# Performance work log

Hardware: AMD Instinct MI355X
Metric: run time of the kernel (lower is better)

Reference implementation:

```python
import jax, jax.numpy as jnp
import numpy as np

N_NODES = 100000
N_EDGES = 3200000
D_FEAT = 128
N_CLASSES = 8


def setup_inputs() -> dict:
    key = jax.random.key(0)
    ks = jax.random.split(key, 8)
    x = jax.random.normal(ks[0], (N_NODES, D_FEAT), dtype=jnp.float32)
    edge_index = jax.random.randint(ks[1], (2, N_EDGES), 0, N_NODES, dtype=jnp.int64)
    W1 = jax.random.normal(ks[2], (D_FEAT, 32), dtype=jnp.float32) / np.sqrt(D_FEAT)
    b1 = jnp.zeros((32,), dtype=jnp.float32)
    W2 = jax.random.normal(ks[3], (32, 16), dtype=jnp.float32) / np.sqrt(32)
    b2 = jnp.zeros((16,), dtype=jnp.float32)
    Wc = jax.random.normal(ks[4], (16, N_CLASSES), dtype=jnp.float32) / np.sqrt(16)
    bc = jnp.zeros((N_CLASSES,), dtype=jnp.float32)
    return {"x": x, "edge_index": edge_index, "W1": W1, "b1": b1,
            "W2": W2, "b2": b2, "Wc": Wc, "bc": bc}


def _gcn_conv(h, src, dst, norm, W, b, num_nodes):
    # PyG GCNConv: linear transform, then sym-normalized scatter-add, then bias
    h = h @ W                                   # [N, out]
    msg = h[src] * norm[:, None]                # [E+N, out] gather + scale
    out = jax.ops.segment_sum(msg, dst, num_segments=num_nodes)
    return out + b


def reference(x, edge_index, W1, b1, W2, b2, Wc, bc):
    num_nodes = x.shape[0]
    loop = jnp.arange(num_nodes, dtype=edge_index.dtype)
    src = jnp.concatenate([edge_index[0], loop])  # add self-loops (PyG default)
    dst = jnp.concatenate([edge_index[1], loop])
    deg = jax.ops.segment_sum(jnp.ones_like(dst, dtype=x.dtype), dst,
                              num_segments=num_nodes)
    dinv = jnp.where(deg > 0, jax.lax.rsqrt(deg), 0.0)
    norm = dinv[src] * dinv[dst]                # symmetric normalization per edge

    h = _gcn_conv(x, src, dst, norm, W1, b1, num_nodes)
    h = jax.nn.relu(h)
    # dropout p=0.5 is identity in eval mode (training=False)
    h = _gcn_conv(h, src, dst, norm, W2, b2, num_nodes)
    h = jax.nn.relu(h)
    logits = h @ Wc + bc
    return jax.nn.log_softmax(logits, axis=1)
```

## Files before the change

kernel.cpp:

```cpp
#include <hip/hip_runtime.h>
#include <math.h>

#define N_NODES 100000
#define N_EDGES 3200000
#define D_FEAT 128
#define H1 32
#define H2 16
#define NC 8

#define NBUCK 391
#define BCAP 12288
#define HCAP 6144
#define EPB 4096
#define EPT 8
#define NSB ((N_EDGES + EPB - 1) / EPB)

#define P_NODES 32
#define P_CAP 3072

typedef short s16x8 __attribute__((ext_vector_type(8)));
typedef float f32x4 __attribute__((ext_vector_type(4)));

__device__ inline unsigned short f2bf(float f) {
    unsigned int u = __float_as_uint(f);
    u += 0x7FFF + ((u >> 16) & 1);
    return (unsigned short)(u >> 16);
}
__device__ inline float bf2f(unsigned short h) {
    return __uint_as_float((unsigned int)h << 16);
}

__device__ inline int wave_scan_incl(int v, int lane) {
#pragma unroll
    for (int off = 1; off < 64; off <<= 1) {
        const int t = __shfl_up(v, off, 64);
        if (lane >= off) v += t;
    }
    return v;
}


__global__ __launch_bounds__(512) void k_pre(const int* __restrict__ ei,
                                             const float* __restrict__ x,
                                             const float* __restrict__ W1,
                                             int* __restrict__ bucket_cursor,
                                             int* __restrict__ ebuf,
                                             unsigned short* __restrict__ y16) {
    __shared__ union {
        struct {
            int hist[NBUCK], lofs[NBUCK], rank[NBUCK], gb[NBUCK], wsum[8], is64;
            int pay[EPB];
            unsigned short pbk[EPB];
        } sc;
        struct {
            unsigned short wf[2 * 4 * 64 * 8];
            float os[8][16][33];
        } gm;
    } u;
    const int tid = threadIdx.x;
    const int lane = tid & 63;
    const int wid = tid >> 6;

    if (blockIdx.x >= NSB) {
        const int gb_ = blockIdx.x - NSB;
        for (int idx = tid; idx < 2 * 4 * 64 * 8; idx += 512) {
            const int j  = idx & 7;
            const int ln = (idx >> 3) & 63;
            const int kk = (idx >> 9) & 3;
            const int nt = idx >> 11;
            const int k = kk * 32 + ((ln >> 4) << 3) + j;
            const int n = nt * 16 + (ln & 15);
            u.gm.wf[idx] = f2bf(W1[k * H1 + n]);
        }
        __syncthreads();
        const int w = tid >> 6;
        const int m = lane & 15;
        const int quad = lane >> 4;
        const int rl = lane >> 2;
        const int seg = lane & 3;
        const s16x8* bf = (const s16x8*)u.gm.wf;
#pragma unroll
        for (int t = 0; t < 2; ++t) {
            const int row0 = (gb_ << 8) + (w * 2 + t) * 16;
            const bool act = (row0 < N_NODES);
            if (act) {
                f32x4 acc0 = {0.f, 0.f, 0.f, 0.f};
                f32x4 acc1 = {0.f, 0.f, 0.f, 0.f};
#pragma unroll
                for (int kk = 0; kk < 4; ++kk) {
                    const float* xp = x + (size_t)(row0 + m) * D_FEAT + kk * 32 + quad * 8;
                    const float4 p0 = ((const float4*)xp)[0];
                    const float4 p1 = ((const float4*)xp)[1];
                    s16x8 a;
                    a[0] = (short)f2bf(p0.x); a[1] = (short)f2bf(p0.y);
                    a[2] = (short)f2bf(p0.z); a[3] = (short)f2bf(p0.w);
                    a[4] = (short)f2bf(p1.x); a[5] = (short)f2bf(p1.y);
                    a[6] = (short)f2bf(p1.z); a[7] = (short)f2bf(p1.w);
                    acc0 = __builtin_amdgcn_mfma_f32_16x16x32_bf16(a, bf[kk * 64 + lane], acc0, 0, 0, 0);
                    acc1 = __builtin_amdgcn_mfma_f32_16x16x32_bf16(a, bf[(4 + kk) * 64 + lane], acc1, 0, 0, 0);
                }
#pragma unroll
                for (int r = 0; r < 4; ++r) {
                    u.gm.os[w][quad * 4 + r][m]      = acc0[r];
                    u.gm.os[w][quad * 4 + r][16 + m] = acc1[r];
                }
            }
            __syncthreads();
            if (act) {
                const int row = row0 + rl;
                const float* p = &u.gm.os[w][rl][seg * 8];
                uint4 o;
                o.x = (unsigned int)f2bf(p[0]) | ((unsigned int)f2bf(p[1]) << 16);
                o.y = (unsigned int)f2bf(p[2]) | ((unsigned int)f2bf(p[3]) << 16);
                o.z = (unsigned int)f2bf(p[4]) | ((unsigned int)f2bf(p[5]) << 16);
                o.w = (unsigned int)f2bf(p[6]) | ((unsigned int)f2bf(p[7]) << 16);
                *(uint4*)(y16 + (size_t)row * 32 + seg * 8) = o;
            }
            __syncthreads();
        }
        return;
    }

    for (int i = tid; i < NBUCK; i += 512) { u.sc.hist[i] = 0; u.sc.rank[i] = 0; }
    if (tid < 64) {
        int v = ei[2 * tid + 1];
#pragma unroll
        for (int off = 1; off < 64; off <<= 1) v |= __shfl_xor(v, off, 64);
        if (tid == 0) u.sc.is64 = (v == 0) ? 1 : 0;
    }
    __syncthreads();
    const int e0 = blockIdx.x * EPB;
    const int n = min(EPB, N_EDGES - e0);
    const bool is64 = (u.sc.is64 != 0);
    int rs[EPT], rd[EPT];
    if (is64) {
#pragma unroll
        for (int k = 0; k < EPT / 2; ++k) {
            const int i = 2 * (tid + k * 512);
            if (i < n) {
                const int e = e0 + i;
                const int4 s = *(const int4*)&ei[2 * e];
                const int4 d = *(const int4*)&ei[2 * N_EDGES + 2 * e];
                rs[2 * k] = s.x; rs[2 * k + 1] = s.z;
                rd[2 * k] = d.x; rd[2 * k + 1] = d.z;
                atomicAdd(&u.sc.hist[d.x >> 8], 1);
                atomicAdd(&u.sc.hist[d.z >> 8], 1);
            }
        }
    } else {
#pragma unroll
        for (int k = 0; k < EPT / 2; ++k) {
            const int i = 2 * (tid + k * 512);
            if (i < n) {
                const int e = e0 + i;
                const int2 s = *(const int2*)&ei[e];
                const int2 d = *(const int2*)&ei[N_EDGES + e];
                rs[2 * k] = s.x; rs[2 * k + 1] = s.y;
                rd[2 * k] = d.x; rd[2 * k + 1] = d.y;
                atomicAdd(&u.sc.hist[d.x >> 8], 1);
                atomicAdd(&u.sc.hist[d.y >> 8], 1);
            }
        }
    }
    __syncthreads();
    const int own = (tid < NBUCK) ? u.sc.hist[tid] : 0;
    int incl = wave_scan_incl(own, lane);
    if (lane == 63) u.sc.wsum[wid] = incl;
    __syncthreads();
    if (tid == 0) {
        int r = 0;
#pragma unroll
        for (int w = 0; w < 8; ++w) { const int t = u.sc.wsum[w]; u.sc.wsum[w] = r; r += t; }
    }
    __syncthreads();
    incl += u.sc.wsum[wid];
    if (tid < NBUCK) {
        u.sc.lofs[tid] = incl - own;
        if (own > 0) u.sc.gb[tid] = tid * BCAP + atomicAdd(&bucket_cursor[tid], own);
    }
    __syncthreads();
#pragma unroll
    for (int k = 0; k < EPT / 2; ++k) {
        const int i = 2 * (tid + k * 512);
        if (i < n) {
#pragma unroll
            for (int j = 0; j < 2; ++j) {
                const int b = rd[2 * k + j] >> 8;
                const int p = u.sc.lofs[b] + atomicAdd(&u.sc.rank[b], 1);
                u.sc.pay[p] = (rs[2 * k + j] << 8) | (rd[2 * k + j] & 255);
                u.sc.pbk[p] = (unsigned short)b;
            }
        }
    }
    __syncthreads();
    for (int p = tid; p < n; p += 512) {
        const int b = u.sc.pbk[p];
        ebuf[u.sc.gb[b] + (p - u.sc.lofs[b])] = u.sc.pay[p];
    }
}


__global__ __launch_bounds__(512) void k_mid(const int* __restrict__ ebuf,
                                             const int* __restrict__ bucket_cursor,
                                             const unsigned short* __restrict__ y16,
                                             int* __restrict__ degc,
                                             float* __restrict__ dinv,
                                             unsigned int* __restrict__ u1q) {
    __shared__ int cnt[256];
    const int b = blockIdx.x;
    const int tid = threadIdx.x;
    if (tid < 256) cnt[tid] = 0;
    __syncthreads();
    const int nb = bucket_cursor[b];
    const int rb = b * BCAP;
    for (int i = tid; i < nb; i += 512)
        atomicAdd(&cnt[ebuf[rb + i] & 255], 1);
    __syncthreads();
    if (tid < 256) {
        const int v = (b << 8) + tid;
        const int cn = cnt[tid];
        degc[v] = cn;
        if (v < N_NODES) {
            const float dv = rsqrtf(1.0f + (float)cn);
            dinv[v] = dv;
            unsigned int r[16];
            const uint4* yp = (const uint4*)(y16 + (size_t)v * 32);
            *(uint4*)&r[0]  = yp[0];
            *(uint4*)&r[4]  = yp[1];
            *(uint4*)&r[8]  = yp[2];
            *(uint4*)&r[12] = yp[3];
            unsigned int wq[8];
#pragma unroll
            for (int j = 0; j < 8; ++j) {
                const float c0 = bf2f((unsigned short)r[2 * j]) * dv;
                const float c1 = bf2f((unsigned short)(r[2 * j] >> 16)) * dv;
                const float c2 = bf2f((unsigned short)r[2 * j + 1]) * dv;
                const float c3 = bf2f((unsigned short)(r[2 * j + 1] >> 16)) * dv;
                unsigned int pk = __builtin_amdgcn_cvt_pk_fp8_f32(c0, c1, 0u, false);
                wq[j] = __builtin_amdgcn_cvt_pk_fp8_f32(c2, c3, pk, true);
            }
            uint4 oa; oa.x = wq[0]; oa.y = wq[1]; oa.z = wq[2]; oa.w = wq[3];
            uint4 ob; ob.x = wq[4]; ob.y = wq[5]; ob.z = wq[6]; ob.w = wq[7];
            ((uint4*)u1q)[(size_t)v * 2]     = oa;
            ((uint4*)u1q)[(size_t)v * 2 + 1] = ob;
        }
    }
}


#define ACC8(Q) do { \
    a0 += __builtin_amdgcn_cvt_f32_fp8((Q).x, 0); \
    a1 += __builtin_amdgcn_cvt_f32_fp8((Q).x, 1); \
    a2 += __builtin_amdgcn_cvt_f32_fp8((Q).x, 2); \
    a3 += __builtin_amdgcn_cvt_f32_fp8((Q).x, 3); \
    a4 += __builtin_amdgcn_cvt_f32_fp8((Q).y, 0); \
    a5 += __builtin_amdgcn_cvt_f32_fp8((Q).y, 1); \
    a6 += __builtin_amdgcn_cvt_f32_fp8((Q).y, 2); \
    a7 += __builtin_amdgcn_cvt_f32_fp8((Q).y, 3); \
} while (0)

__global__ __launch_bounds__(512) void k_fuse1(const int* __restrict__ ebuf,
                                               const int* __restrict__ bucket_cursor,
                                               const int* __restrict__ degc,
                                               const unsigned int* __restrict__ u1q,
                                               const float* __restrict__ b1,
                                               const float* __restrict__ W2,
                                               int* __restrict__ row_ptr,
                                               int* __restrict__ col_idx,
                                               unsigned int* __restrict__ u2b) {
    __shared__ int srt[HCAP];
    __shared__ int cnt[256];
    __shared__ int cur[256];
    __shared__ int wsum[8];
    __shared__ int wsum2[4];
    __shared__ float Ws[H1 * H2];
    __shared__ float hs[128][33];
    __shared__ int s_wb, s_base, s_nh;
    const int b = blockIdx.x >> 1;
    const int h = blockIdx.x & 1;
    const int tid = threadIdx.x;
    const int lane = tid & 63;
    const int wid = tid >> 6;
    if (tid < 256) cnt[tid] = degc[(b << 8) + tid];
    for (int i = tid; i < H1 * H2; i += 512) Ws[i] = W2[i];
    const int own0 = (tid < NBUCK) ? bucket_cursor[tid] : 0;
    int incl0 = wave_scan_incl(own0, lane);
    if (lane == 63) wsum[wid] = incl0;
    __syncthreads();
    if (tid == 0) {
        int r = 0;
#pragma unroll
        for (int w = 0; w < 8; ++w) { const int t = wsum[w]; wsum[w] = r; r += t; }
    }
    __syncthreads();
    if (tid == b) s_wb = incl0 + wsum[wid] - own0;
    const int nb = bucket_cursor[b];
    const int rb = b * BCAP;
    int ownc = 0, inclc = 0;
    if (tid < 256) {
        ownc = cnt[tid];
        inclc = wave_scan_incl(ownc, lane);
        if (lane == 63) wsum2[wid] = inclc;
    }
    __syncthreads();
    if (tid == 0) {
        int r = 0;
#pragma unroll
        for (int w = 0; w < 4; ++w) { const int t = wsum2[w]; wsum2[w] = r; r += t; }
    }
    __syncthreads();
    const int wb = s_wb;
    if (tid < 256) {
        inclc += wsum2[wid];
        const int excl = inclc - ownc;
        cur[tid] = excl;
        const int v = (b << 8) + tid;
        if (v <= N_NODES) row_ptr[v] = wb + excl;
    }
    __syncthreads();
    if (tid == 0) {
        s_base = cur[h * 128];
        s_nh = (h ? nb : cur[128]) - cur[h * 128];
    }
    __syncthreads();
    const int base_h = s_base;
    const int nh = s_nh;
    for (int i = tid; i < nb; i += 512) {
        const int pk = ebuf[rb + i];
        const int dl = pk & 255;
        if ((dl >> 7) == h) {
            const int slot = atomicAdd(&cur[dl], 1);
            srt[slot - base_h] = pk >> 8;
        }
    }
    __syncthreads();
    for (int i = tid; i < nh; i += 512)
        col_idx[wb + base_h + i] = srt[i];
    const int nnl = tid >> 2;
    const int lq = tid & 3;
    const int nn = h * 128 + nnl;
    const int v = (b << 8) + nn;
    if (v < N_NODES) {
        const uint2* base = (const uint2*)u1q;
        const uint2 q = base[(size_t)v * 4 + lq];
        float a0 = __builtin_amdgcn_cvt_f32_fp8(q.x, 0);
        float a1 = __builtin_amdgcn_cvt_f32_fp8(q.x, 1);
        float a2 = __builtin_amdgcn_cvt_f32_fp8(q.x, 2);
        float a3 = __builtin_amdgcn_cvt_f32_fp8(q.x, 3);
        float a4 = __builtin_amdgcn_cvt_f32_fp8(q.y, 0);
        float a5 = __builtin_amdgcn_cvt_f32_fp8(q.y, 1);
        float a6 = __builtin_amdgcn_cvt_f32_fp8(q.y, 2);
        float a7 = __builtin_amdgcn_cvt_f32_fp8(q.y, 3);
        const int cn = cnt[nn];
        const int e = cur[nn] - base_h;
        int j = e - cn;
        for (; j + 7 < e; j += 8) {
            const int s0 = srt[j + 0];
            const int s1 = srt[j + 1];
            const int s2 = srt[j + 2];
            const int s3 = srt[j + 3];
            const int s4 = srt[j + 4];
            const int s5 = srt[j + 5];
            const int s6 = srt[j + 6];
            const int s7 = srt[j + 7];
            const uint2 q0 = base[(size_t)s0 * 4 + lq];
            const uint2 q1 = base[(size_t)s1 * 4 + lq];
            const uint2 q2 = base[(size_t)s2 * 4 + lq];
            const uint2 q3 = base[(size_t)s3 * 4 + lq];
            const uint2 q4 = base[(size_t)s4 * 4 + lq];
            const uint2 q5 = base[(size_t)s5 * 4 + lq];
            const uint2 q6 = base[(size_t)s6 * 4 + lq];
            const uint2 q7 = base[(size_t)s7 * 4 + lq];
            ACC8(q0); ACC8(q1); ACC8(q2); ACC8(q3);
            ACC8(q4); ACC8(q5); ACC8(q6); ACC8(q7);
        }
        for (; j + 3 < e; j += 4) {
            const int s0 = srt[j + 0];
            const int s1 = srt[j + 1];
            const int s2 = srt[j + 2];
            const int s3 = srt[j + 3];
            const uint2 q0 = base[(size_t)s0 * 4 + lq];
            const uint2 q1 = base[(size_t)s1 * 4 + lq];
            const uint2 q2 = base[(size_t)s2 * 4 + lq];
            const uint2 q3 = base[(size_t)s3 * 4 + lq];
            ACC8(q0); ACC8(q1); ACC8(q2); ACC8(q3);
        }
        for (; j < e; ++j) {
            const uint2 qq = base[(size_t)srt[j] * 4 + lq];
            ACC8(qq);
        }
        const float dv = rsqrtf(1.0f + (float)cn);
        const float4 bb0 = ((const float4*)b1)[lq * 2];
        const float4 bb1 = ((const float4*)b1)[lq * 2 + 1];
        float* hp = &hs[nnl][lq * 8];
        hp[0] = fmaxf(fmaf(a0, dv, bb0.x), 0.0f);
        hp[1] = fmaxf(fmaf(a1, dv, bb0.y), 0.0f);
        hp[2] = fmaxf(fmaf(a2, dv, bb0.z), 0.0f);
        hp[3] = fmaxf(fmaf(a3, dv, bb0.w), 0.0f);
        hp[4] = fmaxf(fmaf(a4, dv, bb1.x), 0.0f);
        hp[5] = fmaxf(fmaf(a5, dv, bb1.y), 0.0f);
        hp[6] = fmaxf(fmaf(a6, dv, bb1.z), 0.0f);
        hp[7] = fmaxf(fmaf(a7, dv, bb1.w), 0.0f);
        if (lq == 0) hs[nnl][32] = dv;
    }
    __syncthreads();
    {
        const int nn2 = tid >> 2;
        const int jq = tid & 3;
        const int v2 = (b << 8) + h * 128 + nn2;
        if (v2 < N_NODES) {
            const int j0 = jq * 4;
            const float dv = hs[nn2][32];
            float s0 = 0.f, s1 = 0.f, s2 = 0.f, s3 = 0.f;
#pragma unroll
            for (int k = 0; k < H1; ++k) {
                const float hk = hs[nn2][k];
                s0 = fmaf(hk, Ws[k * H2 + j0 + 0], s0);
                s1 = fmaf(hk, Ws[k * H2 + j0 + 1], s1);
                s2 = fmaf(hk, Ws[k * H2 + j0 + 2], s2);
                s3 = fmaf(hk, Ws[k * H2 + j0 + 3], s3);
            }
            uint2 o;
            o.x = (unsigned int)f2bf(s0 * dv) | ((unsigned int)f2bf(s1 * dv) << 16);
            o.y = (unsigned int)f2bf(s2 * dv) | ((unsigned int)f2bf(s3 * dv) << 16);
            ((uint2*)u2b)[(size_t)v2 * 4 + jq] = o;
        }
    }
}


#define ACC4(Q) do { \
    a0 += bf2f((unsigned short)(Q).x); \
    a1 += bf2f((unsigned short)((Q).x >> 16)); \
    a2 += bf2f((unsigned short)(Q).y); \
    a3 += bf2f((unsigned short)((Q).y >> 16)); \
} while (0)

__global__ __launch_bounds__(256) void k_pull2f(const int* __restrict__ row_ptr,
                                                const int* __restrict__ col_idx,
                                                const float* __restrict__ dinv,
                                                const unsigned int* __restrict__ u2b,
                                                const float* __restrict__ b2,
                                                const float* __restrict__ Wc,
                                                const float* __restrict__ bc,
                                                float* __restrict__ out) {
    __shared__ float hs[P_NODES][17];
    __shared__ float Wcs[H2 * NC];
    __shared__ float bcs[NC];
    __shared__ int lidx[P_CAP];
    const int tid = threadIdx.x;
    if (tid < H2 * NC) Wcs[tid] = Wc[tid];
    if (tid < NC) bcs[tid] = bc[tid];
    const int v0 = blockIdx.x * P_NODES;
    const int base_off = row_ptr[v0];
    const int range = row_ptr[v0 + P_NODES] - base_off;
    const bool ovf = (range > P_CAP);
    const int stg = ovf ? 0 : range;
    for (int j = tid; j < stg; j += 256) lidx[j] = col_idx[base_off + j];
    __syncthreads();
    const int n = tid >> 3;
    const int half = (tid >> 2) & 1;
    const int lq = tid & 3;
    const int v = v0 + n;
    const uint2* base = (const uint2*)u2b;
    float a0 = 0.f, a1 = 0.f, a2 = 0.f, a3 = 0.f;
    if (half == 0) {
        const uint2 q = base[(size_t)v * 4 + lq];
        a0 = bf2f((unsigned short)q.x); a1 = bf2f((unsigned short)(q.x >> 16));
        a2 = bf2f((unsigned short)q.y); a3 = bf2f((unsigned short)(q.y >> 16));
    }
    const int beg = row_ptr[v] - base_off;
    const int end = row_ptr[v + 1] - base_off;
    int i = beg + half;
    if (!ovf) {
        for (; i + 14 < end; i += 16) {
            const int s0 = lidx[i];
            const int s1 = lidx[i + 2];
            const int s2 = lidx[i + 4];
            const int s3 = lidx[i + 6];
            const int s4 = lidx[i + 8];
            const int s5 = lidx[i + 10];
            const int s6 = lidx[i + 12];
            const int s7 = lidx[i + 14];
            const uint2 q0 = base[(size_t)s0 * 4 + lq];
            const uint2 q1 = base[(size_t)s1 * 4 + lq];
            const uint2 q2 = base[(size_t)s2 * 4 + lq];
            const uint2 q3 = base[(size_t)s3 * 4 + lq];
            const uint2 q4 = base[(size_t)s4 * 4 + lq];
            const uint2 q5 = base[(size_t)s5 * 4 + lq];
            const uint2 q6 = base[(size_t)s6 * 4 + lq];
            const uint2 q7 = base[(size_t)s7 * 4 + lq];
            ACC4(q0); ACC4(q1); ACC4(q2); ACC4(q3);
            ACC4(q4); ACC4(q5); ACC4(q6); ACC4(q7);
        }
        for (; i + 6 < end; i += 8) {
            const int s0 = lidx[i];
            const int s1 = lidx[i + 2];
            const int s2 = lidx[i + 4];
            const int s3 = lidx[i + 6];
            const uint2 q0 = base[(size_t)s0 * 4 + lq];
            const uint2 q1 = base[(size_t)s1 * 4 + lq];
            const uint2 q2 = base[(size_t)s2 * 4 + lq];
            const uint2 q3 = base[(size_t)s3 * 4 + lq];
            ACC4(q0); ACC4(q1); ACC4(q2); ACC4(q3);
        }
        for (; i < end; i += 2) {
            const uint2 qq = base[(size_t)lidx[i] * 4 + lq];
            ACC4(qq);
        }
    } else {
        const int* gp = col_idx + base_off;
        for (; i + 14 < end; i += 16) {
            const int s0 = gp[i];
            const int s1 = gp[i + 2];
            const int s2 = gp[i + 4];
            const int s3 = gp[i + 6];
            const int s4 = gp[i + 8];
            const int s5 = gp[i + 10];
            const int s6 = gp[i + 12];
            const int s7 = gp[i + 14];
            const uint2 q0 = base[(size_t)s0 * 4 + lq];
            const uint2 q1 = base[(size_t)s1 * 4 + lq];
            const uint2 q2 = base[(size_t)s2 * 4 + lq];
            const uint2 q3 = base[(size_t)s3 * 4 + lq];
            const uint2 q4 = base[(size_t)s4 * 4 + lq];
            const uint2 q5 = base[(size_t)s5 * 4 + lq];
            const uint2 q6 = base[(size_t)s6 * 4 + lq];
            const uint2 q7 = base[(size_t)s7 * 4 + lq];
            ACC4(q0); ACC4(q1); ACC4(q2); ACC4(q3);
            ACC4(q4); ACC4(q5); ACC4(q6); ACC4(q7);
        }
        for (; i < end; i += 2) {
            const uint2 qq = base[(size_t)gp[i] * 4 + lq];
            ACC4(qq);
        }
    }
    a0 += __shfl_xor(a0, 4, 64); a1 += __shfl_xor(a1, 4, 64);
    a2 += __shfl_xor(a2, 4, 64); a3 += __shfl_xor(a3, 4, 64);
    if (half == 0) {
        const float dv = dinv[v];
        const float4 bb = ((const float4*)b2)[lq];
        float* hp = &hs[n][lq * 4];
        hp[0] = fmaxf(fmaf(a0, dv, bb.x), 0.0f);
        hp[1] = fmaxf(fmaf(a1, dv, bb.y), 0.0f);
        hp[2] = fmaxf(fmaf(a2, dv, bb.z), 0.0f);
        hp[3] = fmaxf(fmaf(a3, dv, bb.w), 0.0f);
    }
    __syncthreads();
    if (tid < P_NODES) {
        const int vv = v0 + tid;
        float lg[NC];
#pragma unroll
        for (int j = 0; j < NC; ++j) lg[j] = bcs[j];
#pragma unroll
        for (int k = 0; k < H2; ++k) {
            const float hk = hs[tid][k];
#pragma unroll
            for (int j = 0; j < NC; ++j)
                lg[j] = fmaf(hk, Wcs[k * NC + j], lg[j]);
        }
        float m = lg[0];
#pragma unroll
        for (int j = 1; j < NC; ++j) m = fmaxf(m, lg[j]);
        float s = 0.0f;
#pragma unroll
        for (int j = 0; j < NC; ++j) s += expf(lg[j] - m);
        const float lse = logf(s) + m;
        float4 o0, o1;
        o0.x = lg[0] - lse; o0.y = lg[1] - lse;
        o0.z = lg[2] - lse; o0.w = lg[3] - lse;
        o1.x = lg[4] - lse; o1.y = lg[5] - lse;
        o1.z = lg[6] - lse; o1.w = lg[7] - lse;
        float4* op = (float4*)(out + (size_t)vv * NC);
        op[0] = o0; op[1] = o1;
    }
}


extern "C" void kernel_launch(void* const* d_in, const int* in_sizes, int n_in,
                              void* d_out, int out_size, void* d_ws, size_t ws_size,
                              hipStream_t stream) {
    const float* x   = (const float*)d_in[0];
    const int*   ei  = (const int*)d_in[1];
    const float* W1  = (const float*)d_in[2];
    const float* b1  = (const float*)d_in[3];
    const float* W2  = (const float*)d_in[4];
    const float* b2  = (const float*)d_in[5];
    const float* Wc  = (const float*)d_in[6];
    const float* bc  = (const float*)d_in[7];
    float* out = (float*)d_out;

    int*   bucket_cursor = (int*)d_ws;
    float* dinv          = (float*)(bucket_cursor + 512);
    int*   degc          = (int*)dinv + 100000;
    int*   row_ptr       = degc + 100096;
    int*   col_idx       = row_ptr + 100016;
    unsigned int* u1q    = (unsigned int*)(col_idx + 3200000);
    unsigned int* u2b    = u1q + 800000;
    int*   ebuf          = (int*)(u2b + 800000);
    unsigned short* y16  = (unsigned short*)col_idx;

    hipMemsetAsync(bucket_cursor, 0, 512 * sizeof(int), stream);
    k_pre <<<NSB + NBUCK, 512, 0, stream>>>(ei, x, W1, bucket_cursor, ebuf, y16);
    k_mid <<<NBUCK, 512, 0, stream>>>(ebuf, bucket_cursor, y16, degc, dinv, u1q);
    k_fuse1<<<NBUCK * 2, 512, 0, stream>>>(ebuf, bucket_cursor, degc, u1q, b1, W2, row_ptr, col_idx, u2b);
    k_pull2f<<<N_NODES / P_NODES, 256, 0, stream>>>(row_ptr, col_idx, dinv, u2b, b2, Wc, bc, out);
}
```

Measured before the change: 201.9 us.

## Split destination buckets to 128 nodes and precompute bucket base offsets once

Edges are now binned into 782 buckets of 128 destination nodes instead of 391 buckets of 256. Each k_fuse1 block then reads only its own bucket, where before two half-blocks each scanned the full 256-node bucket and filtered. The global exclusive scan of bucket sizes moves into a single block of k_mid, replacing the redundant per-block scan in k_fuse1. The cost is a larger shared histogram and two-pass scan in k_pre, plus more scattered atomic bucket appends to global memory.

```diff
diff --git a/kernel.cpp b/kernel.cpp
--- a/kernel.cpp
+++ b/kernel.cpp
@@ -8,8 +8,8 @@
 #define H2 16
 #define NC 8
 
-#define NBUCK 391
-#define BCAP 12288
+#define NB2 782
+#define BCAP2 6144
 #define HCAP 6144
 #define EPB 4096
 #define EPT 8
@@ -48,7 +48,8 @@
                                              unsigned short* __restrict__ y16) {
     __shared__ union {
         struct {
-            int hist[NBUCK], lofs[NBUCK], rank[NBUCK], gb[NBUCK], wsum[8], is64;
+            int hist[NB2], lofs[NB2], rank[NB2], gb[NB2];
+            int wsumA[8], wsumB[8], tot, is64;
             int pay[EPB];
             unsigned short pbk[EPB];
         } sc;
@@ -121,7 +122,7 @@
         return;
     }
 
-    for (int i = tid; i < NBUCK; i += 512) { u.sc.hist[i] = 0; u.sc.rank[i] = 0; }
+    for (int i = tid; i < NB2; i += 512) { u.sc.hist[i] = 0; u.sc.rank[i] = 0; }
     if (tid < 64) {
         int v = ei[2 * tid + 1];
 #pragma unroll
@@ -143,8 +144,8 @@
                 const int4 d = *(const int4*)&ei[2 * N_EDGES + 2 * e];
                 rs[2 * k] = s.x; rs[2 * k + 1] = s.z;
                 rd[2 * k] = d.x; rd[2 * k + 1] = d.z;
-                atomicAdd(&u.sc.hist[d.x >> 8], 1);
-                atomicAdd(&u.sc.hist[d.z >> 8], 1);
+                atomicAdd(&u.sc.hist[d.x >> 7], 1);
+                atomicAdd(&u.sc.hist[d.z >> 7], 1);
             }
         }
     } else {
@@ -157,26 +158,40 @@
                 const int2 d = *(const int2*)&ei[N_EDGES + e];
                 rs[2 * k] = s.x; rs[2 * k + 1] = s.y;
                 rd[2 * k] = d.x; rd[2 * k + 1] = d.y;
-                atomicAdd(&u.sc.hist[d.x >> 8], 1);
-                atomicAdd(&u.sc.hist[d.y >> 8], 1);
+                atomicAdd(&u.sc.hist[d.x >> 7], 1);
+                atomicAdd(&u.sc.hist[d.y >> 7], 1);
             }
         }
     }
     __syncthreads();
-    const int own = (tid < NBUCK) ? u.sc.hist[tid] : 0;
-    int incl = wave_scan_incl(own, lane);
-    if (lane == 63) u.sc.wsum[wid] = incl;
+    const int own0 = u.sc.hist[tid];
+    int incl0 = wave_scan_incl(own0, lane);
+    if (lane == 63) u.sc.wsumA[wid] = incl0;
     __syncthreads();
     if (tid == 0) {
         int r = 0;
 #pragma unroll
-        for (int w = 0; w < 8; ++w) { const int t = u.sc.wsum[w]; u.sc.wsum[w] = r; r += t; }
-    }
-    __syncthreads();
-    incl += u.sc.wsum[wid];
-    if (tid < NBUCK) {
-        u.sc.lofs[tid] = incl - own;
-        if (own > 0) u.sc.gb[tid] = tid * BCAP + atomicAdd(&bucket_cursor[tid], own);
+        for (int w = 0; w < 8; ++w) { const int t = u.sc.wsumA[w]; u.sc.wsumA[w] = r; r += t; }
+        u.sc.tot = r;
+    }
+    __syncthreads();
+    incl0 += u.sc.wsumA[wid];
+    u.sc.lofs[tid] = incl0 - own0;
+    const int own1 = (tid < NB2 - 512) ? u.sc.hist[512 + tid] : 0;
+    int incl1 = wave_scan_incl(own1, lane);
+    if (lane == 63) u.sc.wsumB[wid] = incl1;
+    __syncthreads();
+    if (tid == 0) {
+        int r = 0;
+#pragma unroll
+        for (int w = 0; w < 8; ++w) { const int t = u.sc.wsumB[w]; u.sc.wsumB[w] = r; r += t; }
+    }
+    __syncthreads();
+    incl1 += u.sc.wsumB[wid] + u.sc.tot;
+    if (tid < NB2 - 512) u.sc.lofs[512 + tid] = incl1 - own1;
+    for (int i = tid; i < NB2; i += 512) {
+        const int ownI = u.sc.hist[i];
+        if (ownI > 0) u.sc.gb[i] = i * BCAP2 + atomicAdd(&bucket_cursor[i], ownI);
     }
     __syncthreads();
 #pragma unroll
@@ -185,7 +200,7 @@
         if (i < n) {
 #pragma unroll
             for (int j = 0; j < 2; ++j) {
-                const int b = rd[2 * k + j] >> 8;
+                const int b = rd[2 * k + j] >> 7;
                 const int p = u.sc.lofs[b] + atomicAdd(&u.sc.rank[b], 1);
                 u.sc.pay[p] = (rs[2 * k + j] << 8) | (rd[2 * k + j] & 255);
                 u.sc.pbk[p] = (unsigned short)b;
@@ -205,16 +220,23 @@
                                              const unsigned short* __restrict__ y16,
                                              int* __restrict__ degc,
                                              float* __restrict__ dinv,
+                                             int* __restrict__ bbase,
                                              unsigned int* __restrict__ u1q) {
     __shared__ int cnt[256];
+    __shared__ int wsA[8], wsB[8];
+    __shared__ int tt;
     const int b = blockIdx.x;
     const int tid = threadIdx.x;
     if (tid < 256) cnt[tid] = 0;
     __syncthreads();
-    const int nb = bucket_cursor[b];
-    const int rb = b * BCAP;
-    for (int i = tid; i < nb; i += 512)
-        atomicAdd(&cnt[ebuf[rb + i] & 255], 1);
+#pragma unroll
+    for (int j = 0; j < 2; ++j) {
+        const int b2 = 2 * b + j;
+        const int nbj = bucket_cursor[b2];
+        const int rbj = b2 * BCAP2;
+        for (int i = tid; i < nbj; i += 512)
+            atomicAdd(&cnt[ebuf[rbj + i] & 255], 1);
+    }
     __syncthreads();
     if (tid < 256) {
         const int v = (b << 8) + tid;
@@ -245,6 +267,34 @@
             ((uint4*)u1q)[(size_t)v * 2 + 1] = ob;
         }
     }
+    if (b == 0) {
+        const int lane = tid & 63, wid = tid >> 6;
+        const int o0 = bucket_cursor[tid];
+        int i0 = wave_scan_incl(o0, lane);
+        if (lane == 63) wsA[wid] = i0;
+        __syncthreads();
+        if (tid == 0) {
+            int r = 0;
+#pragma unroll
+            for (int w = 0; w < 8; ++w) { const int t = wsA[w]; wsA[w] = r; r += t; }
+            tt = r;
+        }
+        __syncthreads();
+        i0 += wsA[wid];
+        bbase[tid] = i0 - o0;
+        const int o1 = (tid < NB2 - 512) ? bucket_cursor[512 + tid] : 0;
+        int i1 = wave_scan_incl(o1, lane);
+        if (lane == 63) wsB[wid] = i1;
+        __syncthreads();
+        if (tid == 0) {
+            int r = 0;
+#pragma unroll
+            for (int w = 0; w < 8; ++w) { const int t = wsB[w]; wsB[w] = r; r += t; }
+        }
+        __syncthreads();
+        i1 += wsB[wid] + tt;
+        if (tid < NB2 - 512) bbase[512 + tid] = i1 - o1;
+    }
 }
 
 
@@ -262,6 +312,7 @@
 __global__ __launch_bounds__(512) void k_fuse1(const int* __restrict__ ebuf,
                                                const int* __restrict__ bucket_cursor,
                                                const int* __restrict__ degc,
+                                               const int* __restrict__ bbase,
                                                const unsigned int* __restrict__ u1q,
                                                const float* __restrict__ b1,
                                                const float* __restrict__ W2,
@@ -269,77 +320,47 @@
                                                int* __restrict__ col_idx,
                                                unsigned int* __restrict__ u2b) {
     __shared__ int srt[HCAP];
-    __shared__ int cnt[256];
-    __shared__ int cur[256];
-    __shared__ int wsum[8];
-    __shared__ int wsum2[4];
+    __shared__ int cnt[128];
+    __shared__ int cur[128];
+    __shared__ int wsum2[2];
     __shared__ float Ws[H1 * H2];
     __shared__ float hs[128][33];
-    __shared__ int s_wb, s_base, s_nh;
-    const int b = blockIdx.x >> 1;
-    const int h = blockIdx.x & 1;
+    const int b2 = blockIdx.x;
     const int tid = threadIdx.x;
     const int lane = tid & 63;
     const int wid = tid >> 6;
-    if (tid < 256) cnt[tid] = degc[(b << 8) + tid];
+    if (tid < 128) cnt[tid] = degc[(b2 << 7) + tid];
     for (int i = tid; i < H1 * H2; i += 512) Ws[i] = W2[i];
-    const int own0 = (tid < NBUCK) ? bucket_cursor[tid] : 0;
-    int incl0 = wave_scan_incl(own0, lane);
-    if (lane == 63) wsum[wid] = incl0;
-    __syncthreads();
-    if (tid == 0) {
-        int r = 0;
-#pragma unroll
-        for (int w = 0; w < 8; ++w) { const int t = wsum[w]; wsum[w] = r; r += t; }
-    }
-    __syncthreads();
-    if (tid == b) s_wb = incl0 + wsum[wid] - own0;
-    const int nb = bucket_cursor[b];
-    const int rb = b * BCAP;
+    const int wb = bbase[b2];
+    const int nb = bucket_cursor[b2];
+    const int rb = b2 * BCAP2;
+    __syncthreads();
     int ownc = 0, inclc = 0;
-    if (tid < 256) {
+    if (tid < 128) {
         ownc = cnt[tid];
         inclc = wave_scan_incl(ownc, lane);
         if (lane == 63) wsum2[wid] = inclc;
     }
     __syncthreads();
-    if (tid == 0) {
-        int r = 0;
-#pragma unroll
-        for (int w = 0; w < 4; ++w) { const int t = wsum2[w]; wsum2[w] = r; r += t; }
-    }
-    __syncthreads();
-    const int wb = s_wb;
-    if (tid < 256) {
-        inclc += wsum2[wid];
+    if (tid < 128) {
+        if (wid == 1) inclc += wsum2[0];
         const int excl = inclc - ownc;
         cur[tid] = excl;
-        const int v = (b << 8) + tid;
+        const int v = (b2 << 7) + tid;
         if (v <= N_NODES) row_ptr[v] = wb + excl;
     }
     __syncthreads();
-    if (tid == 0) {
-        s_base = cur[h * 128];
-        s_nh = (h ? nb : cur[128]) - cur[h * 128];
-    }
-    __syncthreads();
-    const int base_h = s_base;
-    const int nh = s_nh;
     for (int i = tid; i < nb; i += 512) {
         const int pk = ebuf[rb + i];
-        const int dl = pk & 255;
-        if ((dl >> 7) == h) {
-            const int slot = atomicAdd(&cur[dl], 1);
-            srt[slot - base_h] = pk >> 8;
-        }
-    }
-    __syncthreads();
-    for (int i = tid; i < nh; i += 512)
-        col_idx[wb + base_h + i] = srt[i];
-    const int nnl = tid >> 2;
+        const int slot = atomicAdd(&cur[pk & 127], 1);
+        srt[slot] = pk >> 8;
+    }
+    __syncthreads();
+    for (int i = tid; i < nb; i += 512)
+        col_idx[wb + i] = srt[i];
+    const int nn = tid >> 2;
     const int lq = tid & 3;
-    const int nn = h * 128 + nnl;
-    const int v = (b << 8) + nn;
+    const int v = (b2 << 7) + nn;
     if (v < N_NODES) {
         const uint2* base = (const uint2*)u1q;
         const uint2 q = base[(size_t)v * 4 + lq];
@@ -352,7 +373,7 @@
         float a6 = __builtin_amdgcn_cvt_f32_fp8(q.y, 2);
         float a7 = __builtin_amdgcn_cvt_f32_fp8(q.y, 3);
         const int cn = cnt[nn];
-        const int e = cur[nn] - base_h;
+        const int e = cur[nn];
         int j = e - cn;
         for (; j + 7 < e; j += 8) {
             const int s0 = srt[j + 0];
@@ -392,7 +413,7 @@
         const float dv = rsqrtf(1.0f + (float)cn);
         const float4 bb0 = ((const float4*)b1)[lq * 2];
         const float4 bb1 = ((const float4*)b1)[lq * 2 + 1];
-        float* hp = &hs[nnl][lq * 8];
+        float* hp = &hs[nn][lq * 8];
         hp[0] = fmaxf(fmaf(a0, dv, bb0.x), 0.0f);
         hp[1] = fmaxf(fmaf(a1, dv, bb0.y), 0.0f);
         hp[2] = fmaxf(fmaf(a2, dv, bb0.z), 0.0f);
@@ -401,13 +422,13 @@
         hp[5] = fmaxf(fmaf(a5, dv, bb1.y), 0.0f);
         hp[6] = fmaxf(fmaf(a6, dv, bb1.z), 0.0f);
         hp[7] = fmaxf(fmaf(a7, dv, bb1.w), 0.0f);
-        if (lq == 0) hs[nnl][32] = dv;
+        if (lq == 0) hs[nn][32] = dv;
     }
     __syncthreads();
     {
         const int nn2 = tid >> 2;
         const int jq = tid & 3;
-        const int v2 = (b << 8) + h * 128 + nn2;
+        const int v2 = (b2 << 7) + nn2;
         if (v2 < N_NODES) {
             const int j0 = jq * 4;
             const float dv = hs[nn2][32];
@@ -591,18 +612,19 @@
     float* out = (float*)d_out;
 
     int*   bucket_cursor = (int*)d_ws;
-    float* dinv          = (float*)(bucket_cursor + 512);
+    float* dinv          = (float*)(bucket_cursor + 1024);
     int*   degc          = (int*)dinv + 100000;
-    int*   row_ptr       = degc + 100096;
+    int*   bbase         = degc + 100096;
+    int*   row_ptr       = bbase + 1024;
     int*   col_idx       = row_ptr + 100016;
     unsigned int* u1q    = (unsigned int*)(col_idx + 3200000);
     unsigned int* u2b    = u1q + 800000;
     int*   ebuf          = (int*)(u2b + 800000);
     unsigned short* y16  = (unsigned short*)col_idx;
 
-    hipMemsetAsync(bucket_cursor, 0, 512 * sizeof(int), stream);
-    k_pre <<<NSB + NBUCK, 512, 0, stream>>>(ei, x, W1, bucket_cursor, ebuf, y16);
-    k_mid <<<NBUCK, 512, 0, stream>>>(ebuf, bucket_cursor, y16, degc, dinv, u1q);
-    k_fuse1<<<NBUCK * 2, 512, 0, stream>>>(ebuf, bucket_cursor, degc, u1q, b1, W2, row_ptr, col_idx, u2b);
+    hipMemsetAsync(bucket_cursor, 0, 1024 * sizeof(int), stream);
+    k_pre <<<NSB + 391, 512, 0, stream>>>(ei, x, W1, bucket_cursor, ebuf, y16);
+    k_mid <<<391, 512, 0, stream>>>(ebuf, bucket_cursor, y16, degc, dinv, bbase, u1q);
+    k_fuse1<<<NB2, 512, 0, stream>>>(ebuf, bucket_cursor, degc, bbase, u1q, b1, W2, row_ptr, col_idx, u2b);
     k_pull2f<<<N_NODES / P_NODES, 256, 0, stream>>>(row_ptr, col_idx, dinv, u2b, b2, Wc, bc, out);
 }
```

After: 200.7 us. No clear change (-0.6%).
